# Kernel optimization log

Hardware: AMD Instinct MI355X
Metric: run time of the kernel (lower is better)

The kernel has to match this reference:

```python
import jax, jax.numpy as jnp
import numpy as np

FFT_LENGTH = 2048
HOP_LENGTH = 512  # window_length // 4, window_length == fft_length


def _hann_periodic(n):
    # tf.signal.hann_window(n, periodic=True)
    return (0.5 - 0.5 * jnp.cos(2.0 * jnp.pi * jnp.arange(n) / n)).astype(jnp.float32)


def setup_inputs() -> dict:
    key = jax.random.key(0)
    k1, k2 = jax.random.split(key)
    B, F, NB = 4, 4000, FFT_LENGTH // 2 + 1
    spec_real = jax.random.normal(k1, (B, F, NB), dtype=jnp.float32)
    spec_imag = jax.random.normal(k2, (B, F, NB), dtype=jnp.float32)
    return {"spec_real": spec_real, "spec_imag": spec_imag}


def reference(spec_real, spec_imag) -> jnp.ndarray:
    fft_length, hop = FFT_LENGTH, HOP_LENGTH
    B, F, _ = spec_real.shape
    window = _hann_periodic(fft_length)  # [N], window_length == fft_length so no padding

    # irfft of the complex spectrogram -> time-domain frames [B, F, N]
    frames = jnp.fft.irfft(spec_real + 1j * spec_imag, n=fft_length).astype(jnp.float32)
    windowed = window * frames  # [B, F, N]

    # overlap-and-add: output length L = (F-1)*hop + N
    L = (F - 1) * hop + fft_length
    idx = (jnp.arange(F) * hop)[:, None] + jnp.arange(fft_length)[None, :]  # [F, N]
    out = jnp.zeros((B, L), jnp.float32).at[:, idx].add(windowed)

    # librosa window_sumsquare: overlap-add of squared window, guard tiny values
    wsq = jnp.zeros((L,), jnp.float32).at[idx].add(window * window)
    tiny = jnp.float32(np.finfo(np.float32).tiny)
    window_sum = jnp.where(wsq > tiny, wsq, jnp.float32(1.0))

    y = out / window_sum
    # center=True: trim fft_length//2 on each side
    half = fft_length // 2
    return y[:, half:L - half]
```

## Files before the change

### kernel.cpp

```cpp
#include <hip/hip_runtime.h>
#include <math.h>

#define NB       1025
#define M        1024
#define FFTN     2048
#define HOP      512
#define NFRAMES  4000
#define BATCH    4
#define OUT_T    2047488
#define R_HOPS   8
#define NPAIR    251
#define PI_F     3.14159265358979323846f

__device__ __forceinline__ float2 cmul(float2 a, float2 b) {
    return make_float2(a.x*b.x - a.y*b.y, a.x*b.y + a.y*b.x);
}
__device__ __forceinline__ float4 cmul4(float4 v, float2 w) {
    return make_float4(v.x*w.x - v.y*w.y, v.x*w.y + v.y*w.x,
                       v.z*w.x - v.w*w.y, v.z*w.y + v.w*w.x);
}
__device__ __forceinline__ float4 f4add(float4 a, float4 b){ return make_float4(a.x+b.x, a.y+b.y, a.z+b.z, a.w+b.w); }
__device__ __forceinline__ float4 f4sub(float4 a, float4 b){ return make_float4(a.x-b.x, a.y-b.y, a.z-b.z, a.w-b.w); }
__device__ __forceinline__ float4 f4addi(float4 a, float4 b){ return make_float4(a.x-b.y, a.y+b.x, a.z-b.w, a.w+b.z); }
__device__ __forceinline__ float4 f4subi(float4 a, float4 b){ return make_float4(a.x+b.y, a.y-b.x, a.z+b.w, a.w-b.z); }

__device__ __forceinline__ int SW4(int i) { return i ^ ((i >> 3) & 7); }

__device__ __forceinline__ float wsq_at(int p) {
    int u  = p + FFTN / 2;
    int fm = u >> 9;
    int n0 = u & 511;
    float wsq = 0.f;
    #pragma unroll
    for (int jj = 0; jj < 4; ++jj) {
        int fr = fm - jj;
        if (fr >= 0 && fr < NFRAMES) {
            int n = n0 + (jj << 9);
            float sw = __sinf((PI_F / (float)FFTN) * (float)n);
            float w  = sw * sw;
            wsq += w * w;
        }
    }
    const float tiny = 1.17549435e-38f;
    return (wsq > tiny) ? wsq : 1.0f;
}
__device__ __forceinline__ float invw_at(int p, bool edge) {
    if (edge && (p < 512 || p >= OUT_T - 512)) return 1.0f / wsq_at(p);
    return (2.0f / 3.0f);
}

template<int ST>
__device__ __forceinline__ void stage4x(const float4* __restrict__ src,
                                        float4* __restrict__ dst, int j, float2 w1) {
    const int Ns = 1 << (2 * ST);
    float4 v0 = src[SW4(j)];
    float4 v1 = src[SW4(j + 256)];
    float4 v2 = src[SW4(j + 512)];
    float4 v3 = src[SW4(j + 768)];
    float2 w2 = cmul(w1, w1);
    float2 w3 = cmul(w2, w1);
    v1 = cmul4(v1, w1); v2 = cmul4(v2, w2); v3 = cmul4(v3, w3);
    float4 t0 = f4add(v0, v2), t1 = f4sub(v0, v2);
    float4 t2 = f4add(v1, v3), t3 = f4sub(v1, v3);
    int jm = j & (Ns - 1);
    int idxD = ((j >> (2 * ST)) << (2 * ST + 2)) + jm;
    dst[SW4(idxD         )] = f4add(t0, t2);
    dst[SW4(idxD +     Ns)] = f4addi(t1, t3);
    dst[SW4(idxD + 2 * Ns)] = f4sub(t0, t2);
    dst[SW4(idxD + 3 * Ns)] = f4subi(t1, t3);
}

__device__ __forceinline__ void load_spec(const float* __restrict__ sr,
                                          const float* __restrict__ si,
                                          int b, int f, int j,
                                          float* car, float* cai,
                                          float* cbr, float* cbi) {
    const size_t fb = ((size_t)b * NFRAMES + f) * NB;
    const float* __restrict__ xr = sr + fb;
    const float* __restrict__ xi = si + fb;
    #pragma unroll
    for (int kk = 0; kk < 4; ++kk) {
        int k  = j + kk * 256;
        int mk = M - k;
        car[kk] = xr[k];  cai[kk] = xi[k];
        cbr[kk] = xr[mk]; cbi[kk] = xi[mk];
    }
}

__device__ __forceinline__ void pack2_st0(float4* __restrict__ dst, int j,
                                          const float2* twp,
                                          const float* a1r, const float* a1i,
                                          const float* b1r, const float* b1i,
                                          const float* a2r, const float* a2i,
                                          const float* b2r, const float* b2i) {
    float4 z[4];
    #pragma unroll
    for (int kk = 0; kk < 4; ++kk) {
        float ar = a1r[kk], ai = a1i[kk], br = b1r[kk], bi = b1i[kk];
        float cr = a2r[kk], ci = a2i[kk], dr = b2r[kk], di = b2i[kk];
        if (kk == 0 && j == 0) { ai = 0.f; bi = 0.f; ci = 0.f; di = 0.f; }
        float2 t = twp[kk];
        float Er = 0.5f*(ar+br), Ei = 0.5f*(ai-bi), Dr = 0.5f*(ar-br), Di = 0.5f*(ai+bi);
        float Or = Dr*t.x - Di*t.y, Oi = Dr*t.y + Di*t.x;
        float Fr = 0.5f*(cr+dr), Fi = 0.5f*(ci-di), Gr = 0.5f*(cr-dr), Gi = 0.5f*(ci+di);
        float Pr = Gr*t.x - Gi*t.y, Pi = Gr*t.y + Gi*t.x;
        z[kk] = make_float4(Er - Oi, Ei + Or, Fr - Pi, Fi + Pr);
    }
    float4 t0 = f4add(z[0], z[2]), t1 = f4sub(z[0], z[2]);
    float4 t2 = f4add(z[1], z[3]), t3 = f4sub(z[1], z[3]);
    dst[SW4(4*j    )] = f4add(t0, t2);
    dst[SW4(4*j + 1)] = f4addi(t1, t3);
    dst[SW4(4*j + 2)] = f4sub(t0, t2);
    dst[SW4(4*j + 3)] = f4subi(t1, t3);
}

__global__ __launch_bounds__(256) void istft_pair_kernel(
    const float* __restrict__ sr, const float* __restrict__ si,
    float* __restrict__ out)
{
    __shared__ float4 buf0[M];
    __shared__ float4 buf1[M];

    const int blk  = blockIdx.x;
    const int b    = blk / NPAIR;
    const int pr   = blk - b * NPAIR;
    const int regA = 2 * pr;
    const int s0hA = regA * R_HOPS;
    const int s0hB = s0hA + R_HOPS;
    const int j    = threadIdx.x;
    const bool edgeA = (regA == 0) || (regA == 500);
    const bool edgeB = (regA + 1 == 500);

    float2 tw_pack[4];
    #pragma unroll
    for (int kk = 0; kk < 4; ++kk) {
        int k = j + kk * 256;
        float s, c;
        __sincosf(PI_F * (float)k * (1.0f / (float)M), &s, &c);
        tw_pack[kk] = make_float2(c, s);
    }
    float2 w1s[4];
    #pragma unroll
    for (int st = 1; st <= 4; ++st) {
        int Ns = 1 << (2 * st);
        int jm = j & (Ns - 1);
        float ang = (0.5f * PI_F / (float)Ns) * (float)jm;
        float s1, c1;
        __sincosf(ang, &s1, &c1);
        w1s[st-1] = make_float2(c1, s1);
    }
    float wreg[4][2];
    #pragma unroll
    for (int q = 0; q < 4; ++q) {
        int n = j + q * 256;
        #pragma unroll
        for (int h = 0; h < 2; ++h) {
            int t = 2 * n + h;
            float swv = __sinf((PI_F / (float)FFTN) * (float)t);
            wreg[q][h] = swv * swv * (1.0f / 1024.0f);
        }
    }

    float2 AccA[R_HOPS], AccB[R_HOPS];
    #pragma unroll
    for (int s = 0; s < R_HOPS; ++s) {
        AccA[s] = make_float2(0.f, 0.f);
        AccB[s] = make_float2(0.f, 0.f);
    }

    #pragma unroll
    for (int it = 0; it < 11; ++it) {
        const int fA = s0hA - 3 + it;
        const int fB = s0hB - 3 + it;
        const bool vA = (fA >= 0) && (fA < NFRAMES);
        const bool vB = (fB >= 0) && (fB < NFRAMES);
        if (!vA && !vB) continue;

        int fAc = fA < 0 ? 0 : (fA > NFRAMES-1 ? NFRAMES-1 : fA);
        int fBc = fB < 0 ? 0 : (fB > NFRAMES-1 ? NFRAMES-1 : fB);

        float a1r[4], a1i[4], b1r[4], b1i[4];
        float a2r[4], a2i[4], b2r[4], b2i[4];
        load_spec(sr, si, b, fAc, j, a1r, a1i, b1r, b1i);
        load_spec(sr, si, b, fBc, j, a2r, a2i, b2r, b2i);

        pack2_st0(buf0, j, tw_pack, a1r, a1i, b1r, b1i, a2r, a2i, b2r, b2i);
        __syncthreads();
        stage4x<1>(buf0, buf1, j, w1s[0]);
        __syncthreads();
        stage4x<2>(buf1, buf0, j, w1s[1]);
        __syncthreads();
        stage4x<3>(buf0, buf1, j, w1s[2]);
        __syncthreads();

        {
            float4 v0 = buf1[SW4(j)];
            float4 v1 = buf1[SW4(j + 256)];
            float4 v2 = buf1[SW4(j + 512)];
            float4 v3 = buf1[SW4(j + 768)];
            float2 w1 = w1s[3];
            float2 w2 = cmul(w1, w1);
            float2 w3 = cmul(w2, w1);
            v1 = cmul4(v1, w1); v2 = cmul4(v2, w2); v3 = cmul4(v3, w3);
            float4 t0 = f4add(v0, v2), t1 = f4sub(v0, v2);
            float4 t2 = f4add(v1, v3), t3 = f4sub(v1, v3);
            float4 g[4];
            g[0] = f4add(t0, t2);
            g[1] = f4addi(t1, t3);
            g[2] = f4sub(t0, t2);
            g[3] = f4subi(t1, t3);
            if (vA) {
                #pragma unroll
                for (int q = 0; q < 4; ++q) {
                    const int s = it - 3 + q;
                    if (s >= 0 && s < R_HOPS) {
                        AccA[s].x += g[q].x * wreg[q][0];
                        AccA[s].y += g[q].y * wreg[q][1];
                    }
                }
            }
            if (vB) {
                #pragma unroll
                for (int q = 0; q < 4; ++q) {
                    const int s = it - 3 + q;
                    if (s >= 0 && s < R_HOPS) {
                        AccB[s].x += g[q].z * wreg[q][0];
                        AccB[s].y += g[q].w * wreg[q][1];
                    }
                }
            }
        }
    }

    float* outb = out + (size_t)b * OUT_T;
    {
        const int base_u = s0hA * HOP;
        #pragma unroll
        for (int s = 0; s < R_HOPS; ++s) {
            int i2 = j + 256 * s;
            int p0 = base_u + 2 * i2 - FFTN / 2;
            int p1 = p0 + 1;
            if ((unsigned)p0 < (unsigned)OUT_T) outb[p0] = AccA[s].x * invw_at(p0, edgeA);
            if ((unsigned)p1 < (unsigned)OUT_T) outb[p1] = AccA[s].y * invw_at(p1, edgeA);
        }
    }
    {
        const int base_u = s0hB * HOP;
        #pragma unroll
        for (int s = 0; s < R_HOPS; ++s) {
            int i2 = j + 256 * s;
            int p0 = base_u + 2 * i2 - FFTN / 2;
            int p1 = p0 + 1;
            if ((unsigned)p0 < (unsigned)OUT_T) outb[p0] = AccB[s].x * invw_at(p0, edgeB);
            if ((unsigned)p1 < (unsigned)OUT_T) outb[p1] = AccB[s].y * invw_at(p1, edgeB);
        }
    }
}

extern "C" void kernel_launch(void* const* d_in, const int* in_sizes, int n_in,
                              void* d_out, int out_size, void* d_ws, size_t ws_size,
                              hipStream_t stream) {
    const float* sr = (const float*)d_in[0];
    const float* si = (const float*)d_in[1];
    float* out = (float*)d_out;
    istft_pair_kernel<<<BATCH * NPAIR, 256, 0, stream>>>(sr, si, out);
}
```

Baseline: 53.78 us.

## Assign one output region per block and pack consecutive frames into the FFT

Measured after the change: 57.40 us. 1.07x slower.

```diff
diff --git a/kernel.cpp b/kernel.cpp
--- a/kernel.cpp
+++ b/kernel.cpp
@@ -9,7 +9,7 @@
 #define BATCH    4
 #define OUT_T    2047488
 #define R_HOPS   8
-#define NPAIR    251
+#define REG_PB   501
 #define PI_F     3.14159265358979323846f
 
 __device__ __forceinline__ float2 cmul(float2 a, float2 b) {
@@ -114,22 +114,19 @@
     dst[SW4(4*j + 3)] = f4subi(t1, t3);
 }
 
-__global__ __launch_bounds__(256) void istft_pair_kernel(
+__global__ __launch_bounds__(256) void istft_rpair_kernel(
     const float* __restrict__ sr, const float* __restrict__ si,
     float* __restrict__ out)
 {
     __shared__ float4 buf0[M];
     __shared__ float4 buf1[M];
 
-    const int blk  = blockIdx.x;
-    const int b    = blk / NPAIR;
-    const int pr   = blk - b * NPAIR;
-    const int regA = 2 * pr;
-    const int s0hA = regA * R_HOPS;
-    const int s0hB = s0hA + R_HOPS;
-    const int j    = threadIdx.x;
-    const bool edgeA = (regA == 0) || (regA == 500);
-    const bool edgeB = (regA + 1 == 500);
+    const int blk = blockIdx.x;
+    const int b   = blk / REG_PB;
+    const int reg = blk - b * REG_PB;
+    const int s0h = reg * R_HOPS;
+    const int j   = threadIdx.x;
+    const bool edge = (reg == 0) || (reg == REG_PB - 1);
 
     float2 tw_pack[4];
     #pragma unroll
@@ -161,19 +158,18 @@
         }
     }
 
-    float2 AccA[R_HOPS], AccB[R_HOPS];
-    #pragma unroll
-    for (int s = 0; s < R_HOPS; ++s) {
-        AccA[s] = make_float2(0.f, 0.f);
-        AccB[s] = make_float2(0.f, 0.f);
-    }
-
-    #pragma unroll
-    for (int it = 0; it < 11; ++it) {
-        const int fA = s0hA - 3 + it;
-        const int fB = s0hB - 3 + it;
+    float2 Acc[R_HOPS];
+    #pragma unroll
+    for (int s = 0; s < R_HOPS; ++s) Acc[s] = make_float2(0.f, 0.f);
+
+    const int fbase = s0h - 3;
+
+    #pragma unroll
+    for (int t = 0; t < 6; ++t) {
+        const int fA = fbase + 2 * t;
+        const int fB = fA + 1;
         const bool vA = (fA >= 0) && (fA < NFRAMES);
-        const bool vB = (fB >= 0) && (fB < NFRAMES);
+        const bool vB = (t < 5) && (fB >= 0) && (fB < NFRAMES);
         if (!vA && !vB) continue;
 
         int fAc = fA < 0 ? 0 : (fA > NFRAMES-1 ? NFRAMES-1 : fA);
@@ -212,20 +208,20 @@
             if (vA) {
                 #pragma unroll
                 for (int q = 0; q < 4; ++q) {
-                    const int s = it - 3 + q;
+                    const int s = 2 * t - 3 + q;
                     if (s >= 0 && s < R_HOPS) {
-                        AccA[s].x += g[q].x * wreg[q][0];
-                        AccA[s].y += g[q].y * wreg[q][1];
+                        Acc[s].x += g[q].x * wreg[q][0];
+                        Acc[s].y += g[q].y * wreg[q][1];
                     }
                 }
             }
             if (vB) {
                 #pragma unroll
                 for (int q = 0; q < 4; ++q) {
-                    const int s = it - 3 + q;
+                    const int s = 2 * t - 2 + q;
                     if (s >= 0 && s < R_HOPS) {
-                        AccB[s].x += g[q].z * wreg[q][0];
-                        AccB[s].y += g[q].w * wreg[q][1];
+                        Acc[s].x += g[q].z * wreg[q][0];
+                        Acc[s].y += g[q].w * wreg[q][1];
                     }
                 }
             }
@@ -233,27 +229,14 @@
     }
 
     float* outb = out + (size_t)b * OUT_T;
-    {
-        const int base_u = s0hA * HOP;
-        #pragma unroll
-        for (int s = 0; s < R_HOPS; ++s) {
-            int i2 = j + 256 * s;
-            int p0 = base_u + 2 * i2 - FFTN / 2;
-            int p1 = p0 + 1;
-            if ((unsigned)p0 < (unsigned)OUT_T) outb[p0] = AccA[s].x * invw_at(p0, edgeA);
-            if ((unsigned)p1 < (unsigned)OUT_T) outb[p1] = AccA[s].y * invw_at(p1, edgeA);
-        }
-    }
-    {
-        const int base_u = s0hB * HOP;
-        #pragma unroll
-        for (int s = 0; s < R_HOPS; ++s) {
-            int i2 = j + 256 * s;
-            int p0 = base_u + 2 * i2 - FFTN / 2;
-            int p1 = p0 + 1;
-            if ((unsigned)p0 < (unsigned)OUT_T) outb[p0] = AccB[s].x * invw_at(p0, edgeB);
-            if ((unsigned)p1 < (unsigned)OUT_T) outb[p1] = AccB[s].y * invw_at(p1, edgeB);
-        }
+    const int base_u = s0h * HOP;
+    #pragma unroll
+    for (int s = 0; s < R_HOPS; ++s) {
+        int i2 = j + 256 * s;
+        int p0 = base_u + 2 * i2 - FFTN / 2;
+        int p1 = p0 + 1;
+        if ((unsigned)p0 < (unsigned)OUT_T) outb[p0] = Acc[s].x * invw_at(p0, edge);
+        if ((unsigned)p1 < (unsigned)OUT_T) outb[p1] = Acc[s].y * invw_at(p1, edge);
     }
 }
 
@@ -263,5 +246,5 @@
     const float* sr = (const float*)d_in[0];
     const float* si = (const float*)d_in[1];
     float* out = (float*)d_out;
-    istft_pair_kernel<<<BATCH * NPAIR, 256, 0, stream>>>(sr, si, out);
-}
+    istft_rpair_kernel<<<BATCH * REG_PB, 256, 0, stream>>>(sr, si, out);
+}
```
